# Kernel optimization log

Measured on AMD Instinct MI355X. Metric: run time of the kernel, lower is better.

## Reference

```python
import jax, jax.numpy as jnp
import numpy as np

N_PAIRS = 1_000_000
N_OBJS = 1000
X_DIM = 48


def setup_inputs() -> dict:
    key = jax.random.key(0)
    ks = jax.random.split(key, 10)
    return {
        "o1": jax.random.randint(ks[0], (N_PAIRS,), 0, N_OBJS, dtype=jnp.int64 if jax.config.jax_enable_x64 else jnp.int32),
        "o2": jax.random.randint(ks[1], (N_PAIRS,), 0, N_OBJS, dtype=jnp.int64 if jax.config.jax_enable_x64 else jnp.int32),
        "T": jax.random.normal(ks[2], (N_PAIRS, 4, 4), dtype=jnp.float32),
        "geoms": jax.random.normal(ks[3], (N_OBJS, X_DIM), dtype=jnp.float32),
        "W1": jax.random.normal(ks[4], (96, 96), dtype=jnp.float32) * 0.1,
        "b1": jax.random.normal(ks[5], (96,), dtype=jnp.float32) * 0.1,
        "W2": jax.random.normal(ks[6], (96, 96), dtype=jnp.float32) * 0.1,
        "b2": jax.random.normal(ks[7], (96,), dtype=jnp.float32) * 0.1,
        "W3": jax.random.normal(ks[8], (96, 1), dtype=jnp.float32) * 0.1,
        "b3": jax.random.normal(ks[9], (1,), dtype=jnp.float32) * 0.1,
    }


def _apply_transforms(x, T):
    # x: [N, D] treated as D//3 3-vectors; homogeneous transform by T [N,4,4].
    N, D = x.shape
    v = x.reshape(N, D // 3, 3)
    # R @ v + t  (equivalent to appending 1 and taking first 3 rows of T)
    out = jnp.einsum('nij,nxj->nxi', T[:, :3, :3], v) + T[:, :3, 3][:, None, :]
    return out.reshape(N, D)


def _mlp(x, W1, b1, W2, b2, W3, b3):
    h = jax.nn.relu(x @ W1 + b1)
    h = jax.nn.relu(h @ W2 + b2)
    return (h @ W3 + b3)[:, 0]  # squeeze -> [N]


def reference(o1, o2, T, geoms, W1, b1, W2, b2, W3, b3):
    x1 = geoms[o1]          # [N, 48]
    x2 = geoms[o2]          # [N, 48]

    def branch(a, b, Tm):
        bt = _apply_transforms(b, Tm)
        x = jnp.concatenate([a, bt], axis=1)  # [N, 96]
        return _mlp(x, W1, b1, W2, b2, W3, b3)

    d_1_2 = branch(x1, x2, T)
    T_inv = jnp.linalg.inv(T)
    d_2_1 = branch(x2, x1, T_inv)
    return 0.5 * (d_1_2 + d_2_1)
```

## Files before the change

### kernel.cpp

```cpp
#include <hip/hip_runtime.h>
#include <hip/hip_bf16.h>

typedef __attribute__((ext_vector_type(8))) short bf16x8;
typedef __attribute__((ext_vector_type(4))) float f32x4;

constexpr int BT   = 1024;
constexpr int KD   = 96;
constexpr int LDX  = 104;
constexpr int LDT  = 12;
constexpr int NBLK = 256;
constexpr int TOTW = NBLK * (BT / 64);

__device__ inline ushort f2bf(float f) {
    uint u = __float_as_uint(f);
    u += 0x7fffu + ((u >> 16) & 1u);
    return (ushort)(u >> 16);
}

__device__ inline uint f2bf2(float lo, float hi) {
    float2 t; t.x = lo; t.y = hi;
    __hip_bfloat162 h = __float22bfloat162_rn(t);
    union { __hip_bfloat162 b; uint u; } cv;
    cv.b = h;
    return cv.u;
}

__global__ void prep_geoms(const float* __restrict__ g, ushort* __restrict__ gb, int n) {
    int i = blockIdx.x * 256 + threadIdx.x;
    if (i < n) gb[i] = f2bf(g[i]);
}

__device__ inline void inv4x4(float4 t0, float4 t1, float4 t2, float4 t3,
                              float* __restrict__ ti) {
    double m00=t0.x, m01=t0.y, m02=t0.z, m03=t0.w;
    double m10=t1.x, m11=t1.y, m12=t1.z, m13=t1.w;
    double m20=t2.x, m21=t2.y, m22=t2.z, m23=t2.w;
    double m30=t3.x, m31=t3.y, m32=t3.z, m33=t3.w;
    double A2323 = m22*m33 - m23*m32;
    double A1323 = m21*m33 - m23*m31;
    double A1223 = m21*m32 - m22*m31;
    double A0323 = m20*m33 - m23*m30;
    double A0223 = m20*m32 - m22*m30;
    double A0123 = m20*m31 - m21*m30;
    double A2313 = m12*m33 - m13*m32;
    double A1313 = m11*m33 - m13*m31;
    double A1213 = m11*m32 - m12*m31;
    double A2312 = m12*m23 - m13*m22;
    double A1312 = m11*m23 - m13*m21;
    double A1212 = m11*m22 - m12*m21;
    double A0313 = m10*m33 - m13*m30;
    double A0213 = m10*m32 - m12*m30;
    double A0312 = m10*m23 - m13*m20;
    double A0212 = m10*m22 - m12*m20;
    double A0113 = m10*m31 - m11*m30;
    double A0112 = m10*m21 - m11*m20;
    double det = m00*(m11*A2323 - m12*A1323 + m13*A1223)
               - m01*(m10*A2323 - m12*A0323 + m13*A0223)
               + m02*(m10*A1323 - m11*A0323 + m13*A0123)
               - m03*(m10*A1223 - m11*A0223 + m12*A0123);
    double idet = 1.0 / det;
    ti[0]  = (float)( idet *  (m11*A2323 - m12*A1323 + m13*A1223) );
    ti[1]  = (float)( idet * -(m01*A2323 - m02*A1323 + m03*A1223) );
    ti[2]  = (float)( idet *  (m01*A2313 - m02*A1313 + m03*A1213) );
    ti[3]  = (float)( idet * -(m01*A2312 - m02*A1312 + m03*A1212) );
    ti[4]  = (float)( idet * -(m10*A2323 - m12*A0323 + m13*A0223) );
    ti[5]  = (float)( idet *  (m00*A2323 - m02*A0323 + m03*A0223) );
    ti[6]  = (float)( idet * -(m00*A2313 - m02*A0313 + m03*A0213) );
    ti[7]  = (float)( idet *  (m00*A2312 - m02*A0312 + m03*A0212) );
    ti[8]  = (float)( idet *  (m10*A1323 - m11*A0323 + m13*A0123) );
    ti[9]  = (float)( idet * -(m00*A1323 - m01*A0323 + m03*A0123) );
    ti[10] = (float)( idet *  (m00*A1313 - m01*A0313 + m03*A0113) );
    ti[11] = (float)( idet * -(m00*A1312 - m01*A0312 + m03*A0112) );
}

__global__ void __launch_bounds__(BT, 4) collision_mfma(
    const int* __restrict__ o1, const int* __restrict__ o2,
    const float* __restrict__ Tg, const float* __restrict__ geoms,
    const ushort* __restrict__ gbf,
    const float* __restrict__ W1, const float* __restrict__ b1,
    const float* __restrict__ W2, const float* __restrict__ b2,
    const float* __restrict__ W3, const float* __restrict__ b3,
    float* __restrict__ out, int N)
{
    __shared__ ushort xs[512 * LDX];
    __shared__ ushort w1t[KD * LDX];
    __shared__ ushort w2t[KD * LDX];
    __shared__ float  tinv[256 * LDT];
    __shared__ float  bls[292];

    const int tid = threadIdx.x;
    const int w   = tid >> 6;
    const int l   = tid & 63;
    const int cl  = l & 15;
    const int g   = l >> 4;
    const int rg  = g * 4;

    const int rl = l & 31;
    const int pt = l >> 5;
    const int br = rl >> 4;
    const int dp = rl & 15;

    for (int i = tid; i < KD * KD; i += BT) {
        int k = i / KD;
        int n = i - k * KD;
        w1t[n * LDX + k] = f2bf(W1[i]);
        w2t[n * LDX + k] = f2bf(W2[i]);
    }
    if (tid < 96) {
        bls[tid]       = b1[tid];
        bls[96 + tid]  = b2[tid];
        bls[192 + tid] = W3[tid];
    }
    if (tid == 96) bls[288] = b3[0];
    __syncthreads();

    const int NWT = N >> 4;
    const int gw  = blockIdx.x * (BT / 64) + w;

    for (int wt = gw; wt < NWT; wt += TOTW) {
        const int pbase = wt * 16;

        if (l < 16) {
            const float4* T4 = reinterpret_cast<const float4*>(Tg + (size_t)(pbase + l) * 16);
            float4 t0 = T4[0], t1 = T4[1], t2 = T4[2], t3 = T4[3];
            inv4x4(t0, t1, t2, t3, &tinv[(w * 16 + l) * LDT]);
        }
        asm volatile("" ::: "memory");

        {
            const int p  = pbase + dp;
            const int ia = o1[p], ib = o2[p];
            const int oa = br ? ib : ia;
            const int ob = br ? ia : ib;
            ushort* xrow = xs + (w * 32 + rl) * LDX;

            {
                const uint4* src = reinterpret_cast<const uint4*>(gbf + oa * 48 + pt * 24);
                uint4* dst = reinterpret_cast<uint4*>(xrow + pt * 24);
                dst[0] = src[0]; dst[1] = src[1]; dst[2] = src[2];
            }

            float4 M0, M1, M2;
            if (br == 0) {
                const float4* Tp = reinterpret_cast<const float4*>(Tg + (size_t)p * 16);
                M0 = Tp[0]; M1 = Tp[1]; M2 = Tp[2];
            } else {
                const float4* t4 = reinterpret_cast<const float4*>(&tinv[(w * 16 + dp) * LDT]);
                M0 = t4[0]; M1 = t4[1]; M2 = t4[2];
            }
            float v[24];
            {
                const float4* bs = reinterpret_cast<const float4*>(geoms + (size_t)ob * 48 + pt * 24);
                #pragma unroll
                for (int q = 0; q < 6; ++q) {
                    float4 t = bs[q];
                    v[4*q+0] = t.x; v[4*q+1] = t.y; v[4*q+2] = t.z; v[4*q+3] = t.w;
                }
            }
            float o[24];
            #pragma unroll
            for (int m = 0; m < 8; ++m) {
                float vx = v[3*m+0], vy = v[3*m+1], vz = v[3*m+2];
                o[3*m+0] = fmaf(M0.x, vx, fmaf(M0.y, vy, fmaf(M0.z, vz, M0.w)));
                o[3*m+1] = fmaf(M1.x, vx, fmaf(M1.y, vy, fmaf(M1.z, vz, M1.w)));
                o[3*m+2] = fmaf(M2.x, vx, fmaf(M2.y, vy, fmaf(M2.z, vz, M2.w)));
            }
            union { uint u[12]; uint4 q4[3]; } pk;
            #pragma unroll
            for (int q = 0; q < 12; ++q)
                pk.u[q] = f2bf2(o[2*q], o[2*q+1]);
            uint4* dst = reinterpret_cast<uint4*>(xrow + 48 + pt * 24);
            dst[0] = pk.q4[0]; dst[1] = pk.q4[1]; dst[2] = pk.q4[2];
        }
        asm volatile("" ::: "memory");

        f32x4 acc[6][2];
        #pragma unroll
        for (int mt = 0; mt < 6; ++mt) {
            f32x4 bv = *reinterpret_cast<const f32x4*>(&bls[mt*16 + rg]);
            acc[mt][0] = bv;
            acc[mt][1] = bv;
        }
        bf16x8 xf[2][3];
        #pragma unroll
        for (int nt = 0; nt < 2; ++nt)
            #pragma unroll
            for (int kb = 0; kb < 3; ++kb)
                xf[nt][kb] = *reinterpret_cast<const bf16x8*>(
                    xs + (w*32 + nt*16 + cl) * LDX + kb*32 + g*8);
        #pragma unroll
        for (int mt = 0; mt < 6; ++mt) {
            bf16x8 wfr[3];
            #pragma unroll
            for (int kb = 0; kb < 3; ++kb)
                wfr[kb] = *reinterpret_cast<const bf16x8*>(
                    w1t + (mt*16 + cl) * LDX + kb*32 + g*8);
            #pragma unroll
            for (int nt = 0; nt < 2; ++nt)
                #pragma unroll
                for (int kb = 0; kb < 3; ++kb)
                    acc[mt][nt] = __builtin_amdgcn_mfma_f32_16x16x32_bf16(
                        wfr[kb], xf[nt][kb], acc[mt][nt], 0, 0, 0);
        }

        #pragma unroll
        for (int mt = 0; mt < 6; ++mt) {
            #pragma unroll
            for (int nt = 0; nt < 2; ++nt) {
                uint2 u2;
                u2.x = f2bf2(fmaxf(acc[mt][nt][0], 0.f), fmaxf(acc[mt][nt][1], 0.f));
                u2.y = f2bf2(fmaxf(acc[mt][nt][2], 0.f), fmaxf(acc[mt][nt][3], 0.f));
                *reinterpret_cast<uint2*>(
                    xs + (w*32 + nt*16 + cl) * LDX + mt*16 + rg) = u2;
            }
        }
        asm volatile("" ::: "memory");

        f32x4 acc2[6][2];
        #pragma unroll
        for (int mt = 0; mt < 6; ++mt) {
            f32x4 bv = *reinterpret_cast<const f32x4*>(&bls[96 + mt*16 + rg]);
            acc2[mt][0] = bv;
            acc2[mt][1] = bv;
        }
        bf16x8 hf[2][3];
        #pragma unroll
        for (int nt = 0; nt < 2; ++nt)
            #pragma unroll
            for (int kb = 0; kb < 3; ++kb)
                hf[nt][kb] = *reinterpret_cast<const bf16x8*>(
                    xs + (w*32 + nt*16 + cl) * LDX + kb*32 + g*8);
        #pragma unroll
        for (int mt = 0; mt < 6; ++mt) {
            bf16x8 wfr[3];
            #pragma unroll
            for (int kb = 0; kb < 3; ++kb)
                wfr[kb] = *reinterpret_cast<const bf16x8*>(
                    w2t + (mt*16 + cl) * LDX + kb*32 + g*8);
            #pragma unroll
            for (int nt = 0; nt < 2; ++nt)
                #pragma unroll
                for (int kb = 0; kb < 3; ++kb)
                    acc2[mt][nt] = __builtin_amdgcn_mfma_f32_16x16x32_bf16(
                        wfr[kb], hf[nt][kb], acc2[mt][nt], 0, 0, 0);
        }

        float pr0 = 0.f, pr1 = 0.f;
        #pragma unroll
        for (int mt = 0; mt < 6; ++mt) {
            f32x4 w3v = *reinterpret_cast<const f32x4*>(&bls[192 + mt*16 + rg]);
            pr0 = fmaf(fmaxf(acc2[mt][0][0], 0.f), w3v[0], pr0);
            pr0 = fmaf(fmaxf(acc2[mt][0][1], 0.f), w3v[1], pr0);
            pr0 = fmaf(fmaxf(acc2[mt][0][2], 0.f), w3v[2], pr0);
            pr0 = fmaf(fmaxf(acc2[mt][0][3], 0.f), w3v[3], pr0);
            pr1 = fmaf(fmaxf(acc2[mt][1][0], 0.f), w3v[0], pr1);
            pr1 = fmaf(fmaxf(acc2[mt][1][1], 0.f), w3v[1], pr1);
            pr1 = fmaf(fmaxf(acc2[mt][1][2], 0.f), w3v[2], pr1);
            pr1 = fmaf(fmaxf(acc2[mt][1][3], 0.f), w3v[3], pr1);
        }
        pr0 += __shfl_xor(pr0, 16, 64);
        pr0 += __shfl_xor(pr0, 32, 64);
        pr1 += __shfl_xor(pr1, 16, 64);
        pr1 += __shfl_xor(pr1, 32, 64);
        if (l < 16)
            out[pbase + l] = 0.5f * (pr0 + pr1) + bls[288];

        asm volatile("" ::: "memory");
    }
}

extern "C" void kernel_launch(void* const* d_in, const int* in_sizes, int n_in,
                              void* d_out, int out_size, void* d_ws, size_t ws_size,
                              hipStream_t stream) {
    const int*   o1    = (const int*)d_in[0];
    const int*   o2    = (const int*)d_in[1];
    const float* T     = (const float*)d_in[2];
    const float* geoms = (const float*)d_in[3];
    const float* W1    = (const float*)d_in[4];
    const float* b1    = (const float*)d_in[5];
    const float* W2    = (const float*)d_in[6];
    const float* b2    = (const float*)d_in[7];
    const float* W3    = (const float*)d_in[8];
    const float* b3    = (const float*)d_in[9];
    float* out = (float*)d_out;
    const int N  = in_sizes[0];
    const int NG = in_sizes[3];

    ushort* gbf = (ushort*)d_ws;
    hipLaunchKernelGGL(prep_geoms, dim3((NG + 255) / 256), dim3(256), 0, stream,
                       geoms, gbf, NG);
    hipLaunchKernelGGL(collision_mfma, dim3(NBLK), dim3(BT), 0, stream,
                       o1, o2, T, geoms, gbf, W1, b1, W2, b2, W3, b3, out, N);
}
```

Before: 133.0 us.

## Process 32 pairs per wave and pre-swizzle weights into MFMA fragment layout

Each wave now handles 32 pairs (four 16-column N tiles) per iteration instead of 16, so each weight fragment loaded from LDS is reused across twice as many MFMAs. The weights are stored in LDS already arranged in per-lane fragment order, which makes the fragment reads contiguous per lane and removes strided transposed reads. The block size drops to 512 threads with a launch-bounds hint of 2 blocks, keeping the xs and tinv buffers the same size. Each wave now holds twice as many accumulators, so register pressure rises and occupancy may fall. The grid still uses 256 blocks, so there are fewer waves in total and each wave runs more iterations.

```diff
diff --git a/kernel.cpp b/kernel.cpp
--- a/kernel.cpp
+++ b/kernel.cpp
@@ -4,7 +4,7 @@
 typedef __attribute__((ext_vector_type(8))) short bf16x8;
 typedef __attribute__((ext_vector_type(4))) float f32x4;
 
-constexpr int BT   = 1024;
+constexpr int BT   = 512;
 constexpr int KD   = 96;
 constexpr int LDX  = 104;
 constexpr int LDT  = 12;
@@ -73,7 +73,7 @@
     ti[11] = (float)( idet * -(m00*A1312 - m01*A0312 + m03*A0112) );
 }
 
-__global__ void __launch_bounds__(BT, 4) collision_mfma(
+__global__ void __launch_bounds__(BT, 2) collision_mfma(
     const int* __restrict__ o1, const int* __restrict__ o2,
     const float* __restrict__ Tg, const float* __restrict__ geoms,
     const ushort* __restrict__ gbf,
@@ -83,8 +83,7 @@
     float* __restrict__ out, int N)
 {
     __shared__ ushort xs[512 * LDX];
-    __shared__ ushort w1t[KD * LDX];
-    __shared__ ushort w2t[KD * LDX];
+    __shared__ ushort wlds[36 * 64 * 8];
     __shared__ float  tinv[256 * LDT];
     __shared__ float  bls[292];
 
@@ -100,11 +99,19 @@
     const int br = rl >> 4;
     const int dp = rl & 15;
 
-    for (int i = tid; i < KD * KD; i += BT) {
-        int k = i / KD;
-        int n = i - k * KD;
-        w1t[n * LDX + k] = f2bf(W1[i]);
-        w2t[n * LDX + k] = f2bf(W2[i]);
+    for (int e = tid; e < 36 * 512; e += BT) {
+        int f    = e >> 9;
+        int r    = e & 511;
+        int lane = r >> 3;
+        int j    = r & 7;
+        int L    = f / 18;
+        int fr   = f - L * 18;
+        int mt   = fr / 3;
+        int kb   = fr - mt * 3;
+        int gg   = lane >> 4;
+        int cc   = lane & 15;
+        const float* W = L ? W2 : W1;
+        wlds[e] = f2bf(W[(kb * 32 + gg * 8 + j) * KD + mt * 16 + cc]);
     }
     if (tid < 96) {
         bls[tid]       = b1[tid];
@@ -114,25 +121,27 @@
     if (tid == 96) bls[288] = b3[0];
     __syncthreads();
 
-    const int NWT = N >> 4;
+    const int NWI = N >> 5;
     const int gw  = blockIdx.x * (BT / 64) + w;
 
-    for (int wt = gw; wt < NWT; wt += TOTW) {
-        const int pbase = wt * 16;
-
-        if (l < 16) {
+    for (int wi = gw; wi < NWI; wi += TOTW) {
+        const int pbase = wi * 32;
+
+        if (l < 32) {
             const float4* T4 = reinterpret_cast<const float4*>(Tg + (size_t)(pbase + l) * 16);
             float4 t0 = T4[0], t1 = T4[1], t2 = T4[2], t3 = T4[3];
-            inv4x4(t0, t1, t2, t3, &tinv[(w * 16 + l) * LDT]);
+            inv4x4(t0, t1, t2, t3, &tinv[(w * 32 + l) * LDT]);
         }
         asm volatile("" ::: "memory");
 
-        {
-            const int p  = pbase + dp;
+        #pragma unroll
+        for (int q = 0; q < 2; ++q) {
+            const int p   = pbase + q * 16 + dp;
+            const int row = q * 32 + rl;
             const int ia = o1[p], ib = o2[p];
             const int oa = br ? ib : ia;
             const int ob = br ? ia : ib;
-            ushort* xrow = xs + (w * 32 + rl) * LDX;
+            ushort* xrow = xs + (w * 64 + row) * LDX;
 
             {
                 const uint4* src = reinterpret_cast<const uint4*>(gbf + oa * 48 + pt * 24);
@@ -145,16 +154,17 @@
                 const float4* Tp = reinterpret_cast<const float4*>(Tg + (size_t)p * 16);
                 M0 = Tp[0]; M1 = Tp[1]; M2 = Tp[2];
             } else {
-                const float4* t4 = reinterpret_cast<const float4*>(&tinv[(w * 16 + dp) * LDT]);
+                const float4* t4 = reinterpret_cast<const float4*>(
+                    &tinv[(w * 32 + q * 16 + dp) * LDT]);
                 M0 = t4[0]; M1 = t4[1]; M2 = t4[2];
             }
             float v[24];
             {
                 const float4* bs = reinterpret_cast<const float4*>(geoms + (size_t)ob * 48 + pt * 24);
                 #pragma unroll
-                for (int q = 0; q < 6; ++q) {
-                    float4 t = bs[q];
-                    v[4*q+0] = t.x; v[4*q+1] = t.y; v[4*q+2] = t.z; v[4*q+3] = t.w;
+                for (int qq = 0; qq < 6; ++qq) {
+                    float4 t = bs[qq];
+                    v[4*qq+0] = t.x; v[4*qq+1] = t.y; v[4*qq+2] = t.z; v[4*qq+3] = t.w;
                 }
             }
             float o[24];
@@ -167,36 +177,36 @@
             }
             union { uint u[12]; uint4 q4[3]; } pk;
             #pragma unroll
-            for (int q = 0; q < 12; ++q)
-                pk.u[q] = f2bf2(o[2*q], o[2*q+1]);
+            for (int qq = 0; qq < 12; ++qq)
+                pk.u[qq] = f2bf2(o[2*qq], o[2*qq+1]);
             uint4* dst = reinterpret_cast<uint4*>(xrow + 48 + pt * 24);
             dst[0] = pk.q4[0]; dst[1] = pk.q4[1]; dst[2] = pk.q4[2];
         }
         asm volatile("" ::: "memory");
 
-        f32x4 acc[6][2];
+        f32x4 acc[6][4];
         #pragma unroll
         for (int mt = 0; mt < 6; ++mt) {
             f32x4 bv = *reinterpret_cast<const f32x4*>(&bls[mt*16 + rg]);
-            acc[mt][0] = bv;
-            acc[mt][1] = bv;
-        }
-        bf16x8 xf[2][3];
-        #pragma unroll
-        for (int nt = 0; nt < 2; ++nt)
+            #pragma unroll
+            for (int nt = 0; nt < 4; ++nt) acc[mt][nt] = bv;
+        }
+        bf16x8 xf[4][3];
+        #pragma unroll
+        for (int nt = 0; nt < 4; ++nt)
             #pragma unroll
             for (int kb = 0; kb < 3; ++kb)
                 xf[nt][kb] = *reinterpret_cast<const bf16x8*>(
-                    xs + (w*32 + nt*16 + cl) * LDX + kb*32 + g*8);
+                    xs + (w*64 + nt*16 + cl) * LDX + kb*32 + g*8);
         #pragma unroll
         for (int mt = 0; mt < 6; ++mt) {
             bf16x8 wfr[3];
             #pragma unroll
             for (int kb = 0; kb < 3; ++kb)
                 wfr[kb] = *reinterpret_cast<const bf16x8*>(
-                    w1t + (mt*16 + cl) * LDX + kb*32 + g*8);
-            #pragma unroll
-            for (int nt = 0; nt < 2; ++nt)
+                    wlds + ((0*18 + mt*3 + kb) * 64 + l) * 8);
+            #pragma unroll
+            for (int nt = 0; nt < 4; ++nt)
                 #pragma unroll
                 for (int kb = 0; kb < 3; ++kb)
                     acc[mt][nt] = __builtin_amdgcn_mfma_f32_16x16x32_bf16(
@@ -206,64 +216,67 @@
         #pragma unroll
         for (int mt = 0; mt < 6; ++mt) {
             #pragma unroll
-            for (int nt = 0; nt < 2; ++nt) {
+            for (int nt = 0; nt < 4; ++nt) {
                 uint2 u2;
                 u2.x = f2bf2(fmaxf(acc[mt][nt][0], 0.f), fmaxf(acc[mt][nt][1], 0.f));
                 u2.y = f2bf2(fmaxf(acc[mt][nt][2], 0.f), fmaxf(acc[mt][nt][3], 0.f));
                 *reinterpret_cast<uint2*>(
-                    xs + (w*32 + nt*16 + cl) * LDX + mt*16 + rg) = u2;
+                    xs + (w*64 + nt*16 + cl) * LDX + mt*16 + rg) = u2;
             }
         }
         asm volatile("" ::: "memory");
 
-        f32x4 acc2[6][2];
+        f32x4 acc2[6][4];
         #pragma unroll
         for (int mt = 0; mt < 6; ++mt) {
             f32x4 bv = *reinterpret_cast<const f32x4*>(&bls[96 + mt*16 + rg]);
-            acc2[mt][0] = bv;
-            acc2[mt][1] = bv;
-        }
-        bf16x8 hf[2][3];
-        #pragma unroll
-        for (int nt = 0; nt < 2; ++nt)
+            #pragma unroll
+            for (int nt = 0; nt < 4; ++nt) acc2[mt][nt] = bv;
+        }
+        bf16x8 hf[4][3];
+        #pragma unroll
+        for (int nt = 0; nt < 4; ++nt)
             #pragma unroll
             for (int kb = 0; kb < 3; ++kb)
                 hf[nt][kb] = *reinterpret_cast<const bf16x8*>(
-                    xs + (w*32 + nt*16 + cl) * LDX + kb*32 + g*8);
+                    xs + (w*64 + nt*16 + cl) * LDX + kb*32 + g*8);
         #pragma unroll
         for (int mt = 0; mt < 6; ++mt) {
             bf16x8 wfr[3];
             #pragma unroll
             for (int kb = 0; kb < 3; ++kb)
                 wfr[kb] = *reinterpret_cast<const bf16x8*>(
-                    w2t + (mt*16 + cl) * LDX + kb*32 + g*8);
-            #pragma unroll
-            for (int nt = 0; nt < 2; ++nt)
+                    wlds + ((1*18 + mt*3 + kb) * 64 + l) * 8);
+            #pragma unroll
+            for (int nt = 0; nt < 4; ++nt)
                 #pragma unroll
                 for (int kb = 0; kb < 3; ++kb)
                     acc2[mt][nt] = __builtin_amdgcn_mfma_f32_16x16x32_bf16(
                         wfr[kb], hf[nt][kb], acc2[mt][nt], 0, 0, 0);
         }
 
-        float pr0 = 0.f, pr1 = 0.f;
+        float pr[4] = {0.f, 0.f, 0.f, 0.f};
         #pragma unroll
         for (int mt = 0; mt < 6; ++mt) {
             f32x4 w3v = *reinterpret_cast<const f32x4*>(&bls[192 + mt*16 + rg]);
-            pr0 = fmaf(fmaxf(acc2[mt][0][0], 0.f), w3v[0], pr0);
-            pr0 = fmaf(fmaxf(acc2[mt][0][1], 0.f), w3v[1], pr0);
-            pr0 = fmaf(fmaxf(acc2[mt][0][2], 0.f), w3v[2], pr0);
-            pr0 = fmaf(fmaxf(acc2[mt][0][3], 0.f), w3v[3], pr0);
-            pr1 = fmaf(fmaxf(acc2[mt][1][0], 0.f), w3v[0], pr1);
-            pr1 = fmaf(fmaxf(acc2[mt][1][1], 0.f), w3v[1], pr1);
-            pr1 = fmaf(fmaxf(acc2[mt][1][2], 0.f), w3v[2], pr1);
-            pr1 = fmaf(fmaxf(acc2[mt][1][3], 0.f), w3v[3], pr1);
-        }
-        pr0 += __shfl_xor(pr0, 16, 64);
-        pr0 += __shfl_xor(pr0, 32, 64);
-        pr1 += __shfl_xor(pr1, 16, 64);
-        pr1 += __shfl_xor(pr1, 32, 64);
-        if (l < 16)
-            out[pbase + l] = 0.5f * (pr0 + pr1) + bls[288];
+            #pragma unroll
+            for (int nt = 0; nt < 4; ++nt) {
+                pr[nt] = fmaf(fmaxf(acc2[mt][nt][0], 0.f), w3v[0], pr[nt]);
+                pr[nt] = fmaf(fmaxf(acc2[mt][nt][1], 0.f), w3v[1], pr[nt]);
+                pr[nt] = fmaf(fmaxf(acc2[mt][nt][2], 0.f), w3v[2], pr[nt]);
+                pr[nt] = fmaf(fmaxf(acc2[mt][nt][3], 0.f), w3v[3], pr[nt]);
+            }
+        }
+        #pragma unroll
+        for (int nt = 0; nt < 4; ++nt) {
+            pr[nt] += __shfl_xor(pr[nt], 16, 64);
+            pr[nt] += __shfl_xor(pr[nt], 32, 64);
+        }
+        if (l < 16) {
+            float b3v = bls[288];
+            out[pbase + l]      = 0.5f * (pr[0] + pr[1]) + b3v;
+            out[pbase + 16 + l] = 0.5f * (pr[2] + pr[3]) + b3v;
+        }
 
         asm volatile("" ::: "memory");
     }
```

After: 137.5 us. +3.3%, slower.
